# Optimization experiments

Measured on AMD Instinct MI355X. Metric: run time of the kernel, lower is better.

Reference implementation:

```python
import jax, jax.numpy as jnp
import numpy as np

DEPTH_CHANNEL = 48  # max_disp(192) / downsample_scale(4)


def setup_inputs() -> dict:
    key = jax.random.key(0)
    k1, k2 = jax.random.split(key)
    B, C, H, W = 4, 512, 96, 312
    left_features = jax.random.normal(k1, (B, C, H, W), dtype=jnp.float32)
    right_features = jax.random.normal(k2, (B, C, H, W), dtype=jnp.float32)
    return {"left_features": left_features, "right_features": right_features}


def reference(left_features, right_features):
    # PSM cosine cost volume: for each disparity i,
    #   cost[:, i, :, i:] = mean_c(left[:, :, :, i:] * right[:, :, :, :W-i])
    # positions w < i remain zero (from the pre-zeroed tensor in the original).
    B, C, H, W = left_features.shape
    planes = []
    for i in range(DEPTH_CHANNEL):  # small fixed disparity loop (48), unrolled under jit
        corr = jnp.mean(
            left_features[:, :, :, i:] * right_features[:, :, :, : W - i],
            axis=1,
        )  # [B, H, W-i]
        planes.append(jnp.pad(corr, ((0, 0), (0, 0), (i, 0))))  # zero-fill w < i
    return jnp.stack(planes, axis=1)  # [B, D, H, W]
```

## Files before the change

kernel.cpp:

```cpp
#include <hip/hip_runtime.h>
#include <hip/hip_bf16.h>
#include <stdint.h>


#define B_ 4
#define C_ 512
#define H_ 96
#define W_ 312
#define D_ 48
#define HW_ (H_ * W_)
#define CHW_ (C_ * HW_)

#define KC 64
#define NCHUNK (C_ / KC)
#define HALFW 156
#define LCOLS 160
#define RCOLS 208
#define PITCH 128
#define LBYTES (LCOLS * PITCH)
#define RBYTES (RCOLS * PITCH)
#define SMEM_BYTES (LBYTES + RBYTES)

#define LITEMS 3
#define RITEMS 4

typedef __bf16 bf16x8 __attribute__((ext_vector_type(8)));
typedef float  f32x4  __attribute__((ext_vector_type(4)));

__device__ __forceinline__ uint32_t pack2_bf16(float a, float b) {
    uint32_t ua = __builtin_bit_cast(uint32_t, a);
    uint32_t ub = __builtin_bit_cast(uint32_t, b);
    ua += 0x7FFFu + ((ua >> 16) & 1u);
    ub += 0x7FFFu + ((ub >> 16) & 1u);
    return (ua >> 16) | (ub & 0xFFFF0000u);
}

__device__ __forceinline__ int lds_slotoff(int lw, int chi) {
    return lw * PITCH + ((chi ^ (lw & 7) ^ ((lw >> 4) & 7)) << 4);
}

__device__ __forceinline__ void lds_barrier() {
    asm volatile("s_waitcnt lgkmcnt(0)" ::: "memory");
    __builtin_amdgcn_s_barrier();
}

__global__ __launch_bounds__(512, 2)
void psm_cost_volume(const float* __restrict__ lf,
                     const float* __restrict__ rf,
                     float* __restrict__ out) {
    const int half = blockIdx.x;
    const int h    = blockIdx.y;
    const int b    = blockIdx.z;
    const int wb   = half * HALFW;
    const int tid  = threadIdx.x;
    const int lane = tid & 63;
    const int wave = tid >> 6;
    const int l15  = lane & 15;
    const int l4   = lane >> 4;
    const int jj   = wave & 3;
    const int nb   = wave >> 2;

    extern __shared__ char smem[];

    const float* lbase = lf + (size_t)b * CHW_ + (size_t)h * W_;
    const float* rbase = rf + (size_t)b * CHW_ + (size_t)h * W_;

    f32x4 acc[5];
    #pragma unroll
    for (int i = 0; i < 5; ++i) acc[i] = f32x4{0.f, 0.f, 0.f, 0.f};

    f32x4 pl0[LITEMS], pl1[LITEMS], pr0[RITEMS], pr1[RITEMS];

    auto LOADS = [&](int c0) {
        #pragma unroll
        for (int it = 0; it < LITEMS; ++it) {
            int idx = tid + it * 512;
            if (idx < 32 * 40) {
                int rp = idx / 40;
                int q  = idx - rp * 40;
                int w4 = wb + 4 * q;
                pl0[it] = f32x4{0.f, 0.f, 0.f, 0.f};
                pl1[it] = f32x4{0.f, 0.f, 0.f, 0.f};
                if (w4 + 3 < W_) {
                    const float* g = lbase + (size_t)(c0 + 2 * rp) * HW_ + w4;
                    pl0[it] = *(const f32x4*)g;
                    pl1[it] = *(const f32x4*)(g + HW_);
                }
            }
        }
        #pragma unroll
        for (int it = 0; it < RITEMS; ++it) {
            int idx = tid + it * 512;
            if (idx < 32 * 52) {
                int rp = idx / 52;
                int q  = idx - rp * 52;
                int w4 = wb - 48 + 4 * q;
                pr0[it] = f32x4{0.f, 0.f, 0.f, 0.f};
                pr1[it] = f32x4{0.f, 0.f, 0.f, 0.f};
                if (w4 >= 0 && w4 + 3 < W_) {
                    const float* g = rbase + (size_t)(c0 + 2 * rp) * HW_ + w4;
                    pr0[it] = *(const f32x4*)g;
                    pr1[it] = *(const f32x4*)(g + HW_);
                }
            }
        }
    };

    auto WRITES = [&]() {
        #pragma unroll
        for (int it = 0; it < LITEMS; ++it) {
            int idx = tid + it * 512;
            if (idx < 32 * 40) {
                int rp  = idx / 40;
                int q   = idx - rp * 40;
                int chi = rp >> 2;
                int cb  = (rp & 3) << 2;
                #pragma unroll
                for (int j = 0; j < 4; ++j) {
                    int lw = 4 * q + j;
                    *(uint32_t*)(smem + lds_slotoff(lw, chi) + cb) =
                        pack2_bf16(pl0[it][j], pl1[it][j]);
                }
            }
        }
        #pragma unroll
        for (int it = 0; it < RITEMS; ++it) {
            int idx = tid + it * 512;
            if (idx < 32 * 52) {
                int rp  = idx / 52;
                int q   = idx - rp * 52;
                int chi = rp >> 2;
                int cb  = (rp & 3) << 2;
                #pragma unroll
                for (int j = 0; j < 4; ++j) {
                    int lw = 4 * q + j;
                    *(uint32_t*)(smem + LBYTES + lds_slotoff(lw, chi) + cb) =
                        pack2_bf16(pr0[it][j], pr1[it][j]);
                }
            }
        }
    };

    LOADS(0);
    for (int ch = 0; ch < NCHUNK; ++ch) {
        if (ch) lds_barrier();
        WRITES();
        if (ch + 1 < NCHUNK) LOADS((ch + 1) * KC);
        lds_barrier();

        #pragma unroll
        for (int ks = 0; ks < 2; ++ks) {
            const int chi = ks * 4 + l4;
            #pragma unroll
            for (int pi = 0; pi < 5; ++pi) {
                const int n   = 2 * pi + nb;
                const int lwB = 16 * n + l15;
                const int lwA = 16 * (n + jj) + l15;
                bf16x8 bfrag = *(const bf16x8*)(smem + lds_slotoff(lwB, chi));
                bf16x8 afrag = *(const bf16x8*)(smem + LBYTES + lds_slotoff(lwA, chi));
                acc[pi] = __builtin_amdgcn_mfma_f32_16x16x32_bf16(afrag, bfrag, acc[pi], 0, 0, 0);
            }
        }
    }
    __syncthreads();

    float* outs = (float*)smem;
    #pragma unroll
    for (int pi = 0; pi < 5; ++pi) {
        const int n  = 2 * pi + nb;
        const int lw = 16 * n + l15;
        #pragma unroll
        for (int r = 0; r < 4; ++r) {
            int tm = 4 * l4 + r;
            int d  = 48 - 16 * jj + l15 - tm;
            if (d >= 0 && d < D_ && lw < HALFW) {
                outs[d * HALFW + lw] = acc[pi][r] * (1.f / 512.f);
            }
        }
    }
    __syncthreads();

    float* obase = out + (size_t)b * (D_ * HW_) + (size_t)h * W_ + wb;
    for (int idx = tid; idx < D_ * HALFW; idx += 512) {
        int d  = idx / HALFW;
        int lw = idx - d * HALFW;
        obase[(size_t)d * HW_ + lw] = outs[idx];
    }
}

extern "C" void kernel_launch(void* const* d_in, const int* in_sizes, int n_in,
                              void* d_out, int out_size, void* d_ws, size_t ws_size,
                              hipStream_t stream) {
    const float* lf = (const float*)d_in[0];
    const float* rf = (const float*)d_in[1];
    float* out = (float*)d_out;
    dim3 grid(2, H_, B_);
    psm_cost_volume<<<grid, 512, SMEM_BYTES, stream>>>(lf, rf, out);
}
```

Baseline: 112.1 us.

## Split each row into four 80-column quarter tiles with 256-thread blocks

Each row is now tiled into four 80-wide column quarters handled by 256-thread blocks, instead of two 156-wide halves handled by 512-thread blocks. The grid grows fourfold, giving better load balance and occupancy across the CUs, and shared memory per block shrinks. The cost is more redundant loading of the right-feature halo (48 extra columns per quarter) and a padded last quarter that covers columns beyond W and has to be masked.

```diff
diff --git a/kernel.cpp b/kernel.cpp
--- a/kernel.cpp
+++ b/kernel.cpp
@@ -13,14 +13,16 @@
 
 #define KC 64
 #define NCHUNK (C_ / KC)
-#define HALFW 156
-#define LCOLS 160
-#define RCOLS 208
+#define NQ 4
+#define QW 80
+#define LCOLS 80
+#define RCOLS 128
 #define PITCH 128
 #define LBYTES (LCOLS * PITCH)
 #define RBYTES (RCOLS * PITCH)
 #define SMEM_BYTES (LBYTES + RBYTES)
 
+#define THREADS 256
 #define LITEMS 3
 #define RITEMS 4
 
@@ -44,21 +46,19 @@
     __builtin_amdgcn_s_barrier();
 }
 
-__global__ __launch_bounds__(512, 2)
+__global__ __launch_bounds__(THREADS, 4)
 void psm_cost_volume(const float* __restrict__ lf,
                      const float* __restrict__ rf,
                      float* __restrict__ out) {
-    const int half = blockIdx.x;
+    const int wq   = blockIdx.x * QW;
     const int h    = blockIdx.y;
     const int b    = blockIdx.z;
-    const int wb   = half * HALFW;
     const int tid  = threadIdx.x;
     const int lane = tid & 63;
     const int wave = tid >> 6;
     const int l15  = lane & 15;
     const int l4   = lane >> 4;
-    const int jj   = wave & 3;
-    const int nb   = wave >> 2;
+    const int jj   = wave;
 
     extern __shared__ char smem[];
 
@@ -74,11 +74,11 @@
     auto LOADS = [&](int c0) {
         #pragma unroll
         for (int it = 0; it < LITEMS; ++it) {
-            int idx = tid + it * 512;
-            if (idx < 32 * 40) {
-                int rp = idx / 40;
-                int q  = idx - rp * 40;
-                int w4 = wb + 4 * q;
+            int idx = tid + it * THREADS;
+            if (idx < 32 * 20) {
+                int rp = idx / 20;
+                int q  = idx - rp * 20;
+                int w4 = wq + 4 * q;
                 pl0[it] = f32x4{0.f, 0.f, 0.f, 0.f};
                 pl1[it] = f32x4{0.f, 0.f, 0.f, 0.f};
                 if (w4 + 3 < W_) {
@@ -90,18 +90,16 @@
         }
         #pragma unroll
         for (int it = 0; it < RITEMS; ++it) {
-            int idx = tid + it * 512;
-            if (idx < 32 * 52) {
-                int rp = idx / 52;
-                int q  = idx - rp * 52;
-                int w4 = wb - 48 + 4 * q;
-                pr0[it] = f32x4{0.f, 0.f, 0.f, 0.f};
-                pr1[it] = f32x4{0.f, 0.f, 0.f, 0.f};
-                if (w4 >= 0 && w4 + 3 < W_) {
-                    const float* g = rbase + (size_t)(c0 + 2 * rp) * HW_ + w4;
-                    pr0[it] = *(const f32x4*)g;
-                    pr1[it] = *(const f32x4*)(g + HW_);
-                }
+            int idx = tid + it * THREADS;
+            int rp  = idx >> 5;
+            int q   = idx & 31;
+            int w4  = wq - 48 + 4 * q;
+            pr0[it] = f32x4{0.f, 0.f, 0.f, 0.f};
+            pr1[it] = f32x4{0.f, 0.f, 0.f, 0.f};
+            if (w4 >= 0 && w4 + 3 < W_) {
+                const float* g = rbase + (size_t)(c0 + 2 * rp) * HW_ + w4;
+                pr0[it] = *(const f32x4*)g;
+                pr1[it] = *(const f32x4*)(g + HW_);
             }
         }
     };
@@ -109,10 +107,10 @@
     auto WRITES = [&]() {
         #pragma unroll
         for (int it = 0; it < LITEMS; ++it) {
-            int idx = tid + it * 512;
-            if (idx < 32 * 40) {
-                int rp  = idx / 40;
-                int q   = idx - rp * 40;
+            int idx = tid + it * THREADS;
+            if (idx < 32 * 20) {
+                int rp  = idx / 20;
+                int q   = idx - rp * 20;
                 int chi = rp >> 2;
                 int cb  = (rp & 3) << 2;
                 #pragma unroll
@@ -125,18 +123,16 @@
         }
         #pragma unroll
         for (int it = 0; it < RITEMS; ++it) {
-            int idx = tid + it * 512;
-            if (idx < 32 * 52) {
-                int rp  = idx / 52;
-                int q   = idx - rp * 52;
-                int chi = rp >> 2;
-                int cb  = (rp & 3) << 2;
-                #pragma unroll
-                for (int j = 0; j < 4; ++j) {
-                    int lw = 4 * q + j;
-                    *(uint32_t*)(smem + LBYTES + lds_slotoff(lw, chi) + cb) =
-                        pack2_bf16(pr0[it][j], pr1[it][j]);
-                }
+            int idx = tid + it * THREADS;
+            int rp  = idx >> 5;
+            int q   = idx & 31;
+            int chi = rp >> 2;
+            int cb  = (rp & 3) << 2;
+            #pragma unroll
+            for (int j = 0; j < 4; ++j) {
+                int lw = 4 * q + j;
+                *(uint32_t*)(smem + LBYTES + lds_slotoff(lw, chi) + cb) =
+                    pack2_bf16(pr0[it][j], pr1[it][j]);
             }
         }
     };
@@ -153,9 +149,8 @@
             const int chi = ks * 4 + l4;
             #pragma unroll
             for (int pi = 0; pi < 5; ++pi) {
-                const int n   = 2 * pi + nb;
-                const int lwB = 16 * n + l15;
-                const int lwA = 16 * (n + jj) + l15;
+                const int lwB = 16 * pi + l15;
+                const int lwA = 16 * (pi + jj) + l15;
                 bf16x8 bfrag = *(const bf16x8*)(smem + lds_slotoff(lwB, chi));
                 bf16x8 afrag = *(const bf16x8*)(smem + LBYTES + lds_slotoff(lwA, chi));
                 acc[pi] = __builtin_amdgcn_mfma_f32_16x16x32_bf16(afrag, bfrag, acc[pi], 0, 0, 0);
@@ -167,24 +162,27 @@
     float* outs = (float*)smem;
     #pragma unroll
     for (int pi = 0; pi < 5; ++pi) {
-        const int n  = 2 * pi + nb;
-        const int lw = 16 * n + l15;
+        const int lw = 16 * pi + l15;
         #pragma unroll
         for (int r = 0; r < 4; ++r) {
             int tm = 4 * l4 + r;
             int d  = 48 - 16 * jj + l15 - tm;
-            if (d >= 0 && d < D_ && lw < HALFW) {
-                outs[d * HALFW + lw] = acc[pi][r] * (1.f / 512.f);
+            if (d >= 0 && d < D_) {
+                outs[d * QW + lw] = acc[pi][r] * (1.f / 512.f);
             }
         }
     }
     __syncthreads();
 
-    float* obase = out + (size_t)b * (D_ * HW_) + (size_t)h * W_ + wb;
-    for (int idx = tid; idx < D_ * HALFW; idx += 512) {
-        int d  = idx / HALFW;
-        int lw = idx - d * HALFW;
-        obase[(size_t)d * HW_ + lw] = outs[idx];
+    float* obase = out + (size_t)b * (D_ * HW_) + (size_t)h * W_ + wq;
+    #pragma unroll
+    for (int it = 0; it < (D_ * QW) / THREADS; ++it) {
+        int idx = it * THREADS + tid;
+        int d   = idx / QW;
+        int lw  = idx - d * QW;
+        if (wq + lw < W_) {
+            obase[(size_t)d * HW_ + lw] = outs[idx];
+        }
     }
 }
 
@@ -194,6 +192,6 @@
     const float* lf = (const float*)d_in[0];
     const float* rf = (const float*)d_in[1];
     float* out = (float*)d_out;
-    dim3 grid(2, H_, B_);
-    psm_cost_volume<<<grid, 512, SMEM_BYTES, stream>>>(lf, rf, out);
+    dim3 grid(NQ, H_, B_);
+    psm_cost_volume<<<grid, THREADS, SMEM_BYTES, stream>>>(lf, rf, out);
 }
```

Result: slower. 190.1 us (+69.5%).
